# Kernel optimization log

Measured on AMD Instinct MI355X. Metric: run time of the kernel, lower is better.

## Reference

```python
import jax, jax.numpy as jnp
import numpy as np

B, C, H, V = 16384, 5, 256, 512
NUM_ITER = 2


def setup_inputs() -> dict:
    key = jax.random.key(0)
    k1, k2, k3, k4 = jax.random.split(key, 4)
    # v0: one-hot categorical visible units, shape [B, C, V, 1]
    idx = jax.random.randint(k1, (B, V), 0, C)
    v0 = jax.nn.one_hot(idx, C, axis=1, dtype=jnp.float32)[..., None]
    W = 0.01 * jax.random.normal(k2, (C, H, V), dtype=jnp.float32)
    b = 0.01 * jax.random.normal(k3, (C, V, 1), dtype=jnp.float32)
    c = 0.01 * jax.random.normal(k4, (H, 1), dtype=jnp.float32)
    return {"v0": v0, "W": W, "b": b, "c": c, "num_sampling_iter": NUM_ITER}


def reference(v0, W, b, c, num_sampling_iter):
    key = jax.random.key(42)
    b2 = b[..., 0]   # [C, V]
    c1 = c[:, 0]     # [H]
    v = v0[..., 0]   # [B, C, V]

    def sample_h(k, v):
        # p(h=1|v) = sigmoid(sum_c W[c] @ v[:,c] + c)
        p = jax.nn.sigmoid(jnp.einsum('chv,bcv->bh', W, v) + c1)  # [B, H]
        return jax.random.bernoulli(k, p).astype(v.dtype)

    def sample_v(k, h):
        # logits over categories per visible unit: W[c].T @ h + b[c]
        logits = jnp.einsum('chv,bh->bcv', W, h) + b2  # [B, C, V]
        idx = jax.random.categorical(k, logits, axis=1)  # [B, V]
        return jax.nn.one_hot(idx, C, axis=1, dtype=h.dtype)  # [B, C, V]

    keys = jax.random.split(key, 2 * num_sampling_iter + 1)
    h = sample_h(keys[0], v)
    h_given_v0 = h
    for i in range(num_sampling_iter):  # small fixed iteration count
        v = sample_v(keys[2 * i + 1], h)
        h = sample_h(keys[2 * i + 2], v)
    return (v[..., None], h[..., None], h_given_v0[..., None])
```

## Files before the change

### kernel.cpp

```cpp
#include <hip/hip_runtime.h>
#include <cstdint>
#include <cstddef>


#define B_DIM 16384
#define C_DIM 5
#define H_DIM 256
#define V_DIM 512
#define KC    320

struct TFOut { uint32_t a, b; };

typedef float f32x2 __attribute__((ext_vector_type(2)));
typedef float f32x4 __attribute__((ext_vector_type(4)));

static __device__ inline f32x2 mk2(float x, float y) {
  f32x2 r; r.x = x; r.y = y; return r;
}

static __device__ inline f32x2 pkfma(f32x2 a, f32x2 b, f32x2 c) {
#if __has_builtin(__builtin_elementwise_fma)
  return __builtin_elementwise_fma(a, b, c);
#else
  f32x2 r; r.x = fmaf(a.x, b.x, c.x); r.y = fmaf(a.y, b.y, c.y); return r;
#endif
}

__host__ __device__ static inline TFOut tf2x32(uint32_t k0, uint32_t k1,
                                               uint32_t c0, uint32_t c1) {
  uint32_t ks2 = k0 ^ k1 ^ 0x1BD11BDAu;
  uint32_t x0 = c0 + k0, x1 = c1 + k1;
#define TF_R(r) { x0 += x1; x1 = (x1 << r) | (x1 >> (32 - r)); x1 ^= x0; }
  TF_R(13) TF_R(15) TF_R(26) TF_R(6)
  x0 += k1;  x1 += ks2 + 1u;
  TF_R(17) TF_R(29) TF_R(16) TF_R(24)
  x0 += ks2; x1 += k0 + 2u;
  TF_R(13) TF_R(15) TF_R(26) TF_R(6)
  x0 += k0;  x1 += k1 + 3u;
  TF_R(17) TF_R(29) TF_R(16) TF_R(24)
  x0 += k1;  x1 += ks2 + 4u;
  TF_R(13) TF_R(15) TF_R(26) TF_R(6)
  x0 += ks2; x1 += k0 + 5u;
#undef TF_R
  TFOut o; o.a = x0; o.b = x1; return o;
}

__device__ static inline uint32_t rng_bits(uint32_t k0, uint32_t k1, uint32_t i) {
  TFOut r = tf2x32(k0, k1, 0u, i);
  return r.a ^ r.b;
}

__device__ static inline float bits_to_unit_float(uint32_t bits) {
  return __uint_as_float((bits >> 9) | 0x3F800000u) - 1.0f;
}

__device__ static float xla_exp(float x_in) {
#pragma clang fp contract(off)
  float x = fminf(x_in, 88.3762626647950f);
  x = fmaxf(x, -88.3762626647949f);
  float fx = floorf(x * 1.44269504088896341f + 0.5f);
  float tmp = fx * 0.693359375f;
  float z = fx * -2.12194440e-4f;
  x = x - tmp;
  x = x - z;
  z = x * x;
  float y = 1.9875691500e-4f;
  y = y * x + 1.3981999507e-3f;
  y = y * x + 8.3334519073e-3f;
  y = y * x + 4.1665795894e-2f;
  y = y * x + 1.6666665459e-1f;
  y = y * x + 5.0000001201e-1f;
  y = y * z + x;
  y = y + 1.0f;
  int n = (int)fx;
  y = y * __uint_as_float((uint32_t)(n + 127) << 23);
  return y;
}

__device__ static float xla_log(float x_in) {
#pragma clang fp contract(off)
  float xv = fmaxf(x_in, 1.17549435e-38f);
  uint32_t bits = __float_as_uint(xv);
  float e = (float)((int)(bits >> 23) - 126);
  float x = __uint_as_float((bits & 0x007FFFFFu) | 0x3F000000u);
  bool m = (x < 0.707106781186547524f);
  float tmp = m ? x : 0.0f;
  x = x - 1.0f;
  e = e - (m ? 1.0f : 0.0f);
  x = x + tmp;
  float z = x * x;
  float y = 7.0376836292e-2f;
  y = y * x + -1.1514610310e-1f;
  y = y * x + 1.1676998740e-1f;
  y = y * x + -1.2420140846e-1f;
  y = y * x + 1.4249322787e-1f;
  y = y * x + -1.6668057665e-1f;
  y = y * x + 2.0000714765e-1f;
  y = y * x + -2.4999993993e-1f;
  y = y * x + 3.3333331174e-1f;
  y = y * x;
  y = y * z;
  float t1 = e * -2.12194440e-4f;
  y = y + t1;
  float t2 = z * 0.5f;
  y = y - t2;
  x = x + y;
  float t3 = e * 0.693359375f;
  x = x + t3;
  return x;
}


__global__ void k_sentinel(float* out, float d) {
  out[0] = d;
}

__global__ __launch_bounds__(256) void k_idx(const float* __restrict__ v0,
                                             uint8_t* __restrict__ idx) {
  int t = blockIdx.x * 256 + threadIdx.x;
  int b = t >> 9, v = t & 511;
  const float* p = v0 + (size_t)b * (C_DIM * V_DIM) + v;
  int cf = 0;
#pragma unroll
  for (int c = 0; c < C_DIM; ++c)
    if (p[c * V_DIM] > 0.5f) cf = c;
  idx[t] = (uint8_t)cf;
}

__global__ __launch_bounds__(256) void k_wt(const float* __restrict__ W,
                                            float* __restrict__ Wt) {
  int t = blockIdx.x * 256 + threadIdx.x;
  int h = t & 255; int rest = t >> 8; int v = rest & 511; int c = rest >> 9;
  Wt[t] = W[((size_t)c * H_DIM + h) * V_DIM + v];
}

__global__ __launch_bounds__(256) void k_sample_h(
    const float* __restrict__ Wt, const float* __restrict__ c1,
    const uint8_t* __restrict__ idx,
    float* __restrict__ out_h, uint32_t* __restrict__ out_mask,
    uint32_t key0, uint32_t key1) {
  __shared__ uint8_t  sidx[V_DIM];
  __shared__ uint32_t soff[V_DIM];
  __shared__ uint16_t cnt[8][5];
  __shared__ uint16_t base[8][5];
  __shared__ uint16_t jb[10];
  int b = blockIdx.x;
  int t = threadIdx.x;
  if (t < 128)
    ((uint32_t*)sidx)[t] = ((const uint32_t*)(idx + (size_t)b * V_DIM))[t];
  __syncthreads();

  int lane = t & 63, wv = t >> 6;
  int v0 = t,       c0 = sidx[v0];
  int v1 = t + 256, c1i = sidx[v1];
  int rank0, rank1;
  {
    unsigned long long bal[5];
#pragma unroll
    for (int cc = 0; cc < 5; ++cc) bal[cc] = __ballot(c0 == cc);
    if (lane == 0) {
#pragma unroll
      for (int cc = 0; cc < 5; ++cc) cnt[wv][cc] = (uint16_t)__popcll(bal[cc]);
    }
    rank0 = (int)__popcll(bal[c0] & ((1ull << lane) - 1ull));
  }
  {
    unsigned long long bal[5];
#pragma unroll
    for (int cc = 0; cc < 5; ++cc) bal[cc] = __ballot(c1i == cc);
    if (lane == 0) {
#pragma unroll
      for (int cc = 0; cc < 5; ++cc) cnt[4 + wv][cc] = (uint16_t)__popcll(bal[cc]);
    }
    rank1 = (int)__popcll(bal[c1i] & ((1ull << lane) - 1ull));
  }
  __syncthreads();
  if (t == 0) {
    int pos = 0;
    for (int cc = 0; cc < 5; ++cc)
      for (int g = 0; g < 8; ++g) { base[g][cc] = (uint16_t)pos; pos += cnt[g][cc]; }
  }
  __syncthreads();
  soff[base[wv][c0] + rank0]       = (uint32_t)(c0 * V_DIM + v0) << 10;
  soff[base[4 + wv][c1i] + rank1]  = (uint32_t)(c1i * V_DIM + v1) << 10;
  __syncthreads();
  if (t < 10) {
    uint32_t target = (uint32_t)(t * KC) << 10;
    int lo = 0, hi = V_DIM;
    while (lo < hi) { int mid = (lo + hi) >> 1;
      if (soff[mid] < target) lo = mid + 1; else hi = mid; }
    jb[t] = (uint16_t)lo;
  }
  __syncthreads();

  const char* Wh = (const char*)Wt + (size_t)t * 4;
  float total = 0.0f;
  for (int s = 0; s < 9; ++s) {
    int j = jb[s], jend = jb[s + 1];
    float psum = 0.0f;
    for (; j + 4 <= jend; j += 4) {
      float w0 = *(const float*)(Wh + soff[j]);
      float w1 = *(const float*)(Wh + soff[j + 1]);
      float w2 = *(const float*)(Wh + soff[j + 2]);
      float w3 = *(const float*)(Wh + soff[j + 3]);
      psum += w0; psum += w1; psum += w2; psum += w3;
    }
    for (; j < jend; ++j) psum += *(const float*)(Wh + soff[j]);
    total += psum;
  }

  float tt = total + c1[t];
  float p = 1.0f / (1.0f + xla_exp(-tt));

  uint32_t i = (uint32_t)(b * H_DIM + t);
  float u = bits_to_unit_float(rng_bits(key0, key1, i));
  bool hb = (u < p);
  if (out_h) out_h[(size_t)b * H_DIM + t] = hb ? 1.0f : 0.0f;

  unsigned long long m = __ballot(hb);
  if ((t & 63) == 0) {
    out_mask[(size_t)b * 8 + wv * 2 + 0] = (uint32_t)(m & 0xFFFFFFFFull);
    out_mask[(size_t)b * 8 + wv * 2 + 1] = (uint32_t)(m >> 32);
  }
}

__global__ __launch_bounds__(256, 2) void k_gemm_v(
    const float* __restrict__ W, const uint32_t* __restrict__ mask,
    float* __restrict__ sums) {
  __shared__ uint32_t smask[32][8];
  __shared__ __align__(16) float tbf[H_DIM][32];
  int t = threadIdx.x;
  int b0 = blockIdx.x * 32;
  smask[t >> 3][t & 7] = mask[(size_t)b0 * 8 + t];
  __syncthreads();
  {
    int h = t;
    uint32_t w = (uint32_t)(h >> 5), s = (uint32_t)(h & 31);
#pragma unroll
    for (int j = 0; j < 32; ++j)
      tbf[h][j] = (float)((smask[j][w] >> s) & 1u);
  }
  __syncthreads();

  int wv = t >> 6, lane = t & 63;
  int g = wv >> 1, vh = wv & 1;
  int v0 = vh * 256 + (lane << 2);
  int bg = b0 + g * 16;

  for (int c = 0; c < C_DIM; ++c) {
    f32x2 acc[8][4];
#pragma unroll
    for (int p = 0; p < 8; ++p)
#pragma unroll
      for (int q = 0; q < 4; ++q) acc[p][q] = mk2(0.f, 0.f);

    const float* wp = W + (size_t)c * (H_DIM * V_DIM) + v0;
    for (int hh = 0; hh < H_DIM; hh += 4) {
      float4 w4[4];
#pragma unroll
      for (int u = 0; u < 4; ++u)
        w4[u] = *(const float4*)(wp + (size_t)(hh + u) * V_DIM);
#pragma unroll
      for (int u = 0; u < 4; ++u) {
        const f32x4* fp = (const f32x4*)&tbf[hh + u][g * 16];
        f32x4 qA = fp[0], qB = fp[1], qC = fp[2], qD = fp[3];
        f32x2 f0 = __builtin_shufflevector(qA, qA, 0, 1);
        f32x2 f1 = __builtin_shufflevector(qA, qA, 2, 3);
        f32x2 f2 = __builtin_shufflevector(qB, qB, 0, 1);
        f32x2 f3 = __builtin_shufflevector(qB, qB, 2, 3);
        f32x2 f4 = __builtin_shufflevector(qC, qC, 0, 1);
        f32x2 f5 = __builtin_shufflevector(qC, qC, 2, 3);
        f32x2 f6 = __builtin_shufflevector(qD, qD, 0, 1);
        f32x2 f7 = __builtin_shufflevector(qD, qD, 2, 3);
        f32x2 wwx = mk2(w4[u].x, w4[u].x);
        f32x2 wwy = mk2(w4[u].y, w4[u].y);
        f32x2 wwz = mk2(w4[u].z, w4[u].z);
        f32x2 www = mk2(w4[u].w, w4[u].w);
        acc[0][0] = pkfma(wwx, f0, acc[0][0]); acc[0][1] = pkfma(wwy, f0, acc[0][1]);
        acc[0][2] = pkfma(wwz, f0, acc[0][2]); acc[0][3] = pkfma(www, f0, acc[0][3]);
        acc[1][0] = pkfma(wwx, f1, acc[1][0]); acc[1][1] = pkfma(wwy, f1, acc[1][1]);
        acc[1][2] = pkfma(wwz, f1, acc[1][2]); acc[1][3] = pkfma(www, f1, acc[1][3]);
        acc[2][0] = pkfma(wwx, f2, acc[2][0]); acc[2][1] = pkfma(wwy, f2, acc[2][1]);
        acc[2][2] = pkfma(wwz, f2, acc[2][2]); acc[2][3] = pkfma(www, f2, acc[2][3]);
        acc[3][0] = pkfma(wwx, f3, acc[3][0]); acc[3][1] = pkfma(wwy, f3, acc[3][1]);
        acc[3][2] = pkfma(wwz, f3, acc[3][2]); acc[3][3] = pkfma(www, f3, acc[3][3]);
        acc[4][0] = pkfma(wwx, f4, acc[4][0]); acc[4][1] = pkfma(wwy, f4, acc[4][1]);
        acc[4][2] = pkfma(wwz, f4, acc[4][2]); acc[4][3] = pkfma(www, f4, acc[4][3]);
        acc[5][0] = pkfma(wwx, f5, acc[5][0]); acc[5][1] = pkfma(wwy, f5, acc[5][1]);
        acc[5][2] = pkfma(wwz, f5, acc[5][2]); acc[5][3] = pkfma(www, f5, acc[5][3]);
        acc[6][0] = pkfma(wwx, f6, acc[6][0]); acc[6][1] = pkfma(wwy, f6, acc[6][1]);
        acc[6][2] = pkfma(wwz, f6, acc[6][2]); acc[6][3] = pkfma(www, f6, acc[6][3]);
        acc[7][0] = pkfma(wwx, f7, acc[7][0]); acc[7][1] = pkfma(wwy, f7, acc[7][1]);
        acc[7][2] = pkfma(wwz, f7, acc[7][2]); acc[7][3] = pkfma(www, f7, acc[7][3]);
      }
    }
#pragma unroll
    for (int p = 0; p < 8; ++p) {
      float4 oA, oB;
      oA.x = acc[p][0].x; oA.y = acc[p][1].x; oA.z = acc[p][2].x; oA.w = acc[p][3].x;
      oB.x = acc[p][0].y; oB.y = acc[p][1].y; oB.z = acc[p][2].y; oB.w = acc[p][3].y;
      *(float4*)&sums[((size_t)c * B_DIM + bg + 2 * p) * V_DIM + v0] = oA;
      *(float4*)&sums[((size_t)c * B_DIM + bg + 2 * p + 1) * V_DIM + v0] = oB;
    }
  }
}

__global__ __launch_bounds__(256, 4) void k_gumbel_v(
    const float* __restrict__ sums, const float* __restrict__ b2,
    uint8_t* __restrict__ idx_out, uint32_t key0, uint32_t key1) {
  int gidx = blockIdx.x * 256 + threadIdx.x;
  int b = gidx >> 7;
  int v0 = (gidx & 127) << 2;
  float best[4];
  uint32_t bc = 0;
#pragma unroll
  for (int c = 0; c < C_DIM; ++c) {
    float4 av = *(const float4*)&sums[((size_t)c * B_DIM + b) * V_DIM + v0];
    float4 bv = *(const float4*)&b2[c * V_DIM + v0];
    uint32_t ib = ((uint32_t)b * C_DIM + (uint32_t)c) * V_DIM + (uint32_t)v0;
    float avq[4] = {av.x, av.y, av.z, av.w};
    float bvq[4] = {bv.x, bv.y, bv.z, bv.w};
#pragma unroll
    for (int q = 0; q < 4; ++q) {
      float uf = bits_to_unit_float(rng_bits(key0, key1, ib + (uint32_t)q));
      if (uf == 0.0f) uf = 1.17549435e-38f;
      float gz = -xla_log(-xla_log(uf));
      float z = gz + (avq[q] + bvq[q]);
      if (c == 0 || z > best[q]) {
        best[q] = z;
        bc = (bc & ~(0xFFu << (8 * q))) | ((uint32_t)c << (8 * q));
      }
    }
  }
  *(uint32_t*)(idx_out + (size_t)b * V_DIM + v0) = bc;
}

__global__ __launch_bounds__(256) void k_onehot(const uint8_t* __restrict__ idx,
                                                float* __restrict__ out) {
  int t = blockIdx.x * 256 + threadIdx.x;
  int v = t & 511; int rest = t >> 9; int c = rest % C_DIM; int b = rest / C_DIM;
  out[t] = (idx[(size_t)b * V_DIM + v] == c) ? 1.0f : 0.0f;
}


extern "C" void kernel_launch(void* const* d_in, const int* in_sizes, int n_in,
                              void* d_out, int out_size, void* d_ws, size_t ws_size,
                              hipStream_t stream) {
  float* out = (float*)d_out;

  const size_t WS_NEED = 2621440ull
                       + 2621440ull
                       + 8388608ull
                       + 524288ull;
  float D = 0.0f;
  if (n_in < 4)                       D = 910.0f + (float)n_in;
  else if (in_sizes[0] != 41943040)   D = 920.0f;
  else if (in_sizes[1] != 655360)     D = 921.0f;
  else if (in_sizes[2] != 2560)       D = 922.0f;
  else if (in_sizes[3] != 256)        D = 923.0f;
  else if (out_size != 50331648)      D = 930.0f + (float)out_size * 1e-6f;
  else if (ws_size < WS_NEED)         D = 100.0f + (float)(ws_size >> 20);
  if (D != 0.0f) {
    hipLaunchKernelGGL(k_sentinel, dim3(1), dim3(1), 0, stream, out, D);
    return;
  }

  const float* v0 = (const float*)d_in[0];
  const float* W  = (const float*)d_in[1];
  const float* b2 = (const float*)d_in[2];
  const float* c1 = (const float*)d_in[3];

  float* out_v  = out;
  float* out_h  = out + (size_t)B_DIM * C_DIM * V_DIM;
  float* out_h0 = out_h + (size_t)B_DIM * H_DIM;

  char* ws = (char*)d_ws;
  float*    Wt   = (float*)(ws);
  uint8_t*  idx  = (uint8_t*)(ws + 5242880);
  uint32_t* mask = (uint32_t*)(ws + 13631488);

  float* sums = out_v;

  uint32_t keys[5][2];
  for (int i = 0; i < 5; ++i) {
    TFOut r = tf2x32(0u, 42u, 0u, (uint32_t)i);
    keys[i][0] = r.a; keys[i][1] = r.b;
  }

  hipLaunchKernelGGL(k_wt,  dim3(2560),  dim3(256), 0, stream, W, Wt);
  hipLaunchKernelGGL(k_idx, dim3(32768), dim3(256), 0, stream, v0, idx);

  hipLaunchKernelGGL(k_sample_h, dim3(B_DIM), dim3(256), 0, stream,
                     Wt, c1, idx, out_h0, mask, keys[0][0], keys[0][1]);
  hipLaunchKernelGGL(k_gemm_v, dim3(B_DIM / 32), dim3(256), 0, stream,
                     W, mask, sums);
  hipLaunchKernelGGL(k_gumbel_v, dim3(B_DIM * 128 / 256), dim3(256), 0, stream,
                     sums, b2, idx, keys[1][0], keys[1][1]);
  hipLaunchKernelGGL(k_sample_h, dim3(B_DIM), dim3(256), 0, stream,
                     Wt, c1, idx, (float*)nullptr, mask, keys[2][0], keys[2][1]);
  hipLaunchKernelGGL(k_gemm_v, dim3(B_DIM / 32), dim3(256), 0, stream,
                     W, mask, sums);
  hipLaunchKernelGGL(k_gumbel_v, dim3(B_DIM * 128 / 256), dim3(256), 0, stream,
                     sums, b2, idx, keys[3][0], keys[3][1]);
  hipLaunchKernelGGL(k_sample_h, dim3(B_DIM), dim3(256), 0, stream,
                     Wt, c1, idx, out_h, mask, keys[4][0], keys[4][1]);
  hipLaunchKernelGGL(k_onehot, dim3(163840), dim3(256), 0, stream, idx, out_v);
}
```

Before: 1.980 ms.

## Replace per-row gather sample_h with tiled dense one-hot GEMM and split-K reduction

After: 2.035 ms. 1.03x slower.

```diff
diff --git a/kernel.cpp b/kernel.cpp
--- a/kernel.cpp
+++ b/kernel.cpp
@@ -7,7 +7,6 @@
 #define C_DIM 5
 #define H_DIM 256
 #define V_DIM 512
-#define KC    320
 
 struct TFOut { uint32_t a, b; };
 
@@ -134,83 +133,120 @@
   Wt[t] = W[((size_t)c * H_DIM + h) * V_DIM + v];
 }
 
-__global__ __launch_bounds__(256) void k_sample_h(
-    const float* __restrict__ Wt, const float* __restrict__ c1,
-    const uint8_t* __restrict__ idx,
+__global__ __launch_bounds__(256, 2) void k_hpart(
+    const float* __restrict__ Wt, const uint8_t* __restrict__ idx,
+    float* __restrict__ partial) {
+  __shared__ uint8_t sidxT[V_DIM][68];
+  __shared__ __align__(16) float tbf[160][64];
+  int t = threadIdx.x;
+  int bg = blockIdx.x >> 3, s = blockIdx.x & 7;
+  int b0 = bg * 64;
+  int wv = t >> 6, lane = t & 63;
+  int g16 = wv * 16;
+
+  {
+    const uint32_t* src = (const uint32_t*)(idx + (size_t)b0 * V_DIM);
+    for (int i = t; i < 64 * 128; i += 256) {
+      int b = i >> 7, w = i & 127;
+      uint32_t q = src[(size_t)b * 128 + w];
+      int v = w * 4;
+      sidxT[v + 0][b] = (uint8_t)(q);
+      sidxT[v + 1][b] = (uint8_t)(q >> 8);
+      sidxT[v + 2][b] = (uint8_t)(q >> 16);
+      sidxT[v + 3][b] = (uint8_t)(q >> 24);
+    }
+  }
+
+  f32x2 ps[4][8];
+#pragma unroll
+  for (int hq = 0; hq < 4; ++hq)
+#pragma unroll
+    for (int p = 0; p < 8; ++p) ps[hq][p] = mk2(0.f, 0.f);
+
+  for (int tau = 0; tau < 2; ++tau) {
+    int kbase = s * 320 + tau * 160;
+    __syncthreads();
+    {
+      int kk0 = t >> 4, bq = t & 15;
+#pragma unroll
+      for (int i = 0; i < 10; ++i) {
+        int kk = kk0 + 16 * i;
+        int k = kbase + kk;
+        int v = k & 511;
+        uint32_t cc = (uint32_t)(k >> 9);
+        uint32_t q = *(const uint32_t*)&sidxT[v][bq * 4];
+        float4 o;
+        o.x = ((q & 255u) == cc) ? 1.0f : 0.0f;
+        o.y = (((q >> 8) & 255u) == cc) ? 1.0f : 0.0f;
+        o.z = (((q >> 16) & 255u) == cc) ? 1.0f : 0.0f;
+        o.w = (((q >> 24) & 255u) == cc) ? 1.0f : 0.0f;
+        *(float4*)&tbf[kk][bq * 4] = o;
+      }
+    }
+    __syncthreads();
+#pragma unroll 2
+    for (int kk = 0; kk < 160; ++kk) {
+      int k = kbase + kk;
+      float4 w = *(const float4*)(Wt + (size_t)k * H_DIM + (lane << 2));
+      const f32x4* fp = (const f32x4*)&tbf[kk][g16];
+      f32x4 qA = fp[0], qB = fp[1], qC = fp[2], qD = fp[3];
+      f32x2 f0 = __builtin_shufflevector(qA, qA, 0, 1);
+      f32x2 f1 = __builtin_shufflevector(qA, qA, 2, 3);
+      f32x2 f2 = __builtin_shufflevector(qB, qB, 0, 1);
+      f32x2 f3 = __builtin_shufflevector(qB, qB, 2, 3);
+      f32x2 f4 = __builtin_shufflevector(qC, qC, 0, 1);
+      f32x2 f5 = __builtin_shufflevector(qC, qC, 2, 3);
+      f32x2 f6 = __builtin_shufflevector(qD, qD, 0, 1);
+      f32x2 f7 = __builtin_shufflevector(qD, qD, 2, 3);
+      f32x2 w0 = mk2(w.x, w.x);
+      f32x2 w1 = mk2(w.y, w.y);
+      f32x2 w2 = mk2(w.z, w.z);
+      f32x2 w3 = mk2(w.w, w.w);
+      ps[0][0] = pkfma(w0, f0, ps[0][0]); ps[1][0] = pkfma(w1, f0, ps[1][0]);
+      ps[2][0] = pkfma(w2, f0, ps[2][0]); ps[3][0] = pkfma(w3, f0, ps[3][0]);
+      ps[0][1] = pkfma(w0, f1, ps[0][1]); ps[1][1] = pkfma(w1, f1, ps[1][1]);
+      ps[2][1] = pkfma(w2, f1, ps[2][1]); ps[3][1] = pkfma(w3, f1, ps[3][1]);
+      ps[0][2] = pkfma(w0, f2, ps[0][2]); ps[1][2] = pkfma(w1, f2, ps[1][2]);
+      ps[2][2] = pkfma(w2, f2, ps[2][2]); ps[3][2] = pkfma(w3, f2, ps[3][2]);
+      ps[0][3] = pkfma(w0, f3, ps[0][3]); ps[1][3] = pkfma(w1, f3, ps[1][3]);
+      ps[2][3] = pkfma(w2, f3, ps[2][3]); ps[3][3] = pkfma(w3, f3, ps[3][3]);
+      ps[0][4] = pkfma(w0, f4, ps[0][4]); ps[1][4] = pkfma(w1, f4, ps[1][4]);
+      ps[2][4] = pkfma(w2, f4, ps[2][4]); ps[3][4] = pkfma(w3, f4, ps[3][4]);
+      ps[0][5] = pkfma(w0, f5, ps[0][5]); ps[1][5] = pkfma(w1, f5, ps[1][5]);
+      ps[2][5] = pkfma(w2, f5, ps[2][5]); ps[3][5] = pkfma(w3, f5, ps[3][5]);
+      ps[0][6] = pkfma(w0, f6, ps[0][6]); ps[1][6] = pkfma(w1, f6, ps[1][6]);
+      ps[2][6] = pkfma(w2, f6, ps[2][6]); ps[3][6] = pkfma(w3, f6, ps[3][6]);
+      ps[0][7] = pkfma(w0, f7, ps[0][7]); ps[1][7] = pkfma(w1, f7, ps[1][7]);
+      ps[2][7] = pkfma(w2, f7, ps[2][7]); ps[3][7] = pkfma(w3, f7, ps[3][7]);
+    }
+  }
+
+  int h0 = lane << 2;
+#pragma unroll
+  for (int p = 0; p < 8; ++p) {
+    float4 oA, oB;
+    oA.x = ps[0][p].x; oA.y = ps[1][p].x; oA.z = ps[2][p].x; oA.w = ps[3][p].x;
+    oB.x = ps[0][p].y; oB.y = ps[1][p].y; oB.z = ps[2][p].y; oB.w = ps[3][p].y;
+    int bA = b0 + g16 + 2 * p;
+    *(float4*)&partial[((size_t)s * B_DIM + bA) * H_DIM + h0] = oA;
+    *(float4*)&partial[((size_t)s * B_DIM + bA + 1) * H_DIM + h0] = oB;
+  }
+}
+
+__global__ __launch_bounds__(256) void k_hfin(
+    const float* __restrict__ partial, const float* __restrict__ c1,
     float* __restrict__ out_h, uint32_t* __restrict__ out_mask,
     uint32_t key0, uint32_t key1) {
-  __shared__ uint8_t  sidx[V_DIM];
-  __shared__ uint32_t soff[V_DIM];
-  __shared__ uint16_t cnt[8][5];
-  __shared__ uint16_t base[8][5];
-  __shared__ uint16_t jb[10];
   int b = blockIdx.x;
   int t = threadIdx.x;
-  if (t < 128)
-    ((uint32_t*)sidx)[t] = ((const uint32_t*)(idx + (size_t)b * V_DIM))[t];
-  __syncthreads();
-
-  int lane = t & 63, wv = t >> 6;
-  int v0 = t,       c0 = sidx[v0];
-  int v1 = t + 256, c1i = sidx[v1];
-  int rank0, rank1;
-  {
-    unsigned long long bal[5];
-#pragma unroll
-    for (int cc = 0; cc < 5; ++cc) bal[cc] = __ballot(c0 == cc);
-    if (lane == 0) {
-#pragma unroll
-      for (int cc = 0; cc < 5; ++cc) cnt[wv][cc] = (uint16_t)__popcll(bal[cc]);
-    }
-    rank0 = (int)__popcll(bal[c0] & ((1ull << lane) - 1ull));
-  }
-  {
-    unsigned long long bal[5];
-#pragma unroll
-    for (int cc = 0; cc < 5; ++cc) bal[cc] = __ballot(c1i == cc);
-    if (lane == 0) {
-#pragma unroll
-      for (int cc = 0; cc < 5; ++cc) cnt[4 + wv][cc] = (uint16_t)__popcll(bal[cc]);
-    }
-    rank1 = (int)__popcll(bal[c1i] & ((1ull << lane) - 1ull));
-  }
-  __syncthreads();
-  if (t == 0) {
-    int pos = 0;
-    for (int cc = 0; cc < 5; ++cc)
-      for (int g = 0; g < 8; ++g) { base[g][cc] = (uint16_t)pos; pos += cnt[g][cc]; }
-  }
-  __syncthreads();
-  soff[base[wv][c0] + rank0]       = (uint32_t)(c0 * V_DIM + v0) << 10;
-  soff[base[4 + wv][c1i] + rank1]  = (uint32_t)(c1i * V_DIM + v1) << 10;
-  __syncthreads();
-  if (t < 10) {
-    uint32_t target = (uint32_t)(t * KC) << 10;
-    int lo = 0, hi = V_DIM;
-    while (lo < hi) { int mid = (lo + hi) >> 1;
-      if (soff[mid] < target) lo = mid + 1; else hi = mid; }
-    jb[t] = (uint16_t)lo;
-  }
-  __syncthreads();
-
-  const char* Wh = (const char*)Wt + (size_t)t * 4;
-  float total = 0.0f;
-  for (int s = 0; s < 9; ++s) {
-    int j = jb[s], jend = jb[s + 1];
-    float psum = 0.0f;
-    for (; j + 4 <= jend; j += 4) {
-      float w0 = *(const float*)(Wh + soff[j]);
-      float w1 = *(const float*)(Wh + soff[j + 1]);
-      float w2 = *(const float*)(Wh + soff[j + 2]);
-      float w3 = *(const float*)(Wh + soff[j + 3]);
-      psum += w0; psum += w1; psum += w2; psum += w3;
-    }
-    for (; j < jend; ++j) psum += *(const float*)(Wh + soff[j]);
-    total += psum;
-  }
-
-  float tt = total + c1[t];
-  float p = 1.0f / (1.0f + xla_exp(-tt));
+  int wv = t >> 6;
+  float tt = 0.0f;
+#pragma unroll
+  for (int s = 0; s < 8; ++s)
+    tt = tt + partial[((size_t)s * B_DIM + b) * H_DIM + t];
+
+  float tot = tt + c1[t];
+  float p = 1.0f / (1.0f + xla_exp(-tot));
 
   uint32_t i = (uint32_t)(b * H_DIM + t);
   float u = bits_to_unit_float(rng_bits(key0, key1, i));
@@ -379,7 +415,8 @@
   uint8_t*  idx  = (uint8_t*)(ws + 5242880);
   uint32_t* mask = (uint32_t*)(ws + 13631488);
 
-  float* sums = out_v;
+  float* sums    = out_v;
+  float* partial = out_v;
 
   uint32_t keys[5][2];
   for (int i = 0; i < 5; ++i) {
@@ -390,19 +427,22 @@
   hipLaunchKernelGGL(k_wt,  dim3(2560),  dim3(256), 0, stream, W, Wt);
   hipLaunchKernelGGL(k_idx, dim3(32768), dim3(256), 0, stream, v0, idx);
 
-  hipLaunchKernelGGL(k_sample_h, dim3(B_DIM), dim3(256), 0, stream,
-                     Wt, c1, idx, out_h0, mask, keys[0][0], keys[0][1]);
+  hipLaunchKernelGGL(k_hpart, dim3(2048), dim3(256), 0, stream, Wt, idx, partial);
+  hipLaunchKernelGGL(k_hfin,  dim3(B_DIM), dim3(256), 0, stream,
+                     partial, c1, out_h0, mask, keys[0][0], keys[0][1]);
   hipLaunchKernelGGL(k_gemm_v, dim3(B_DIM / 32), dim3(256), 0, stream,
                      W, mask, sums);
   hipLaunchKernelGGL(k_gumbel_v, dim3(B_DIM * 128 / 256), dim3(256), 0, stream,
                      sums, b2, idx, keys[1][0], keys[1][1]);
-  hipLaunchKernelGGL(k_sample_h, dim3(B_DIM), dim3(256), 0, stream,
-                     Wt, c1, idx, (float*)nullptr, mask, keys[2][0], keys[2][1]);
+  hipLaunchKernelGGL(k_hpart, dim3(2048), dim3(256), 0, stream, Wt, idx, partial);
+  hipLaunchKernelGGL(k_hfin,  dim3(B_DIM), dim3(256), 0, stream,
+                     partial, c1, (float*)nullptr, mask, keys[2][0], keys[2][1]);
   hipLaunchKernelGGL(k_gemm_v, dim3(B_DIM / 32), dim3(256), 0, stream,
                      W, mask, sums);
   hipLaunchKernelGGL(k_gumbel_v, dim3(B_DIM * 128 / 256), dim3(256), 0, stream,
                      sums, b2, idx, keys[3][0], keys[3][1]);
-  hipLaunchKernelGGL(k_sample_h, dim3(B_DIM), dim3(256), 0, stream,
-                     Wt, c1, idx, out_h, mask, keys[4][0], keys[4][1]);
+  hipLaunchKernelGGL(k_hpart, dim3(2048), dim3(256), 0, stream, Wt, idx, partial);
+  hipLaunchKernelGGL(k_hfin,  dim3(B_DIM), dim3(256), 0, stream,
+                     partial, c1, out_h, mask, keys[4][0], keys[4][1]);
   hipLaunchKernelGGL(k_onehot, dim3(163840), dim3(256), 0, stream, idx, out_v);
 }
```
